# Optimization experiments

Measured on AMD Instinct MI355X. Metric: run time of the kernel, lower is better.

Reference implementation:

```python
import math
import jax, jax.numpy as jnp
import numpy as np

NUM_BUCKETS = 32
MAX_DISTANCE = 128
N_HEADS = 16
D_KV = 64


def _relative_position_bucket(rel_pos):
    # encoder (bidirectional) path of UMT5Attention._relative_position_bucket
    num_buckets = NUM_BUCKETS // 2
    rel_buckets = (rel_pos > 0).astype(jnp.int32) * num_buckets
    rel_pos = jnp.abs(rel_pos)
    max_exact = num_buckets // 2
    is_small = rel_pos < max_exact
    # clamp to 1 inside log only to avoid nan; those entries are masked by is_small
    rel_pos_large = max_exact + (
        jnp.log(jnp.maximum(rel_pos, 1).astype(jnp.float32) / max_exact)
        / math.log(MAX_DISTANCE / max_exact)
        * (num_buckets - max_exact)
    ).astype(jnp.int32)
    rel_pos_large = jnp.minimum(rel_pos_large, num_buckets - 1)
    return rel_buckets + jnp.where(is_small, rel_pos, rel_pos_large)


def compute_bias(rel_bias, q_len, k_len):
    ctx = jnp.arange(q_len, dtype=jnp.int32)[:, None]
    mem = jnp.arange(k_len, dtype=jnp.int32)[None, :]
    bkt = _relative_position_bucket(mem - ctx)          # [q, k]
    values = rel_bias[bkt]                               # [q, k, H]
    return jnp.transpose(values, (2, 0, 1))[None]        # [1, H, q, k]


def setup_inputs() -> dict:
    key = jax.random.key(0)
    ks = jax.random.split(key, 6)
    B, S, D = 2, 2048, 1024
    s = 1.0 / math.sqrt(D)
    return {
        "hidden_states": jax.random.normal(ks[0], (B, S, D), jnp.float32),
        "attention_mask": jnp.ones((B, S), jnp.int32),
        "Wq": jax.random.normal(ks[1], (D, D), jnp.float32) * s,
        "Wk": jax.random.normal(ks[2], (D, D), jnp.float32) * s,
        "Wv": jax.random.normal(ks[3], (D, D), jnp.float32) * s,
        "Wo": jax.random.normal(ks[4], (D, D), jnp.float32) * s,
        "rel_bias": jax.random.normal(ks[5], (NUM_BUCKETS, N_HEADS), jnp.float32),
    }


def reference(hidden_states, attention_mask, Wq, Wk, Wv, Wo, rel_bias):
    b, s, _ = hidden_states.shape
    n, c = N_HEADS, D_KV
    q = (hidden_states @ Wq).reshape(b, s, n, c)
    k = (hidden_states @ Wk).reshape(b, s, n, c)
    v = (hidden_states @ Wv).reshape(b, s, n, c)
    position_bias = compute_bias(rel_bias, s, s)          # [1, H, s, s]
    mask = attention_mask[:, None, None, :]               # [b, 1, 1, s]
    position_bias = jnp.where(mask == 0,
                              jnp.finfo(hidden_states.dtype).min,
                              position_bias)
    # T5-style: no 1/sqrt(d) query scaling
    attn = jnp.einsum('binc,bjnc->bnij', q, k) + position_bias
    attn = jax.nn.softmax(attn, axis=-1)
    o = jnp.einsum('bnij,bjnc->binc', attn, v).reshape(b, s, n * c)
    return o @ Wo
```

## Files before the change

kernel.cpp:

```cpp
#include <hip/hip_runtime.h>
#include <hip/hip_bf16.h>

#define NH 16
#define DC 64
#define SEQ 2048
#define BATCH 2
#define DM 1024
#define MTOT (BATCH*SEQ)

#define LOG2E 1.44269504f
#define SMAX_BOUND 48.0f

typedef unsigned short u16;
typedef unsigned int u32;
typedef __bf16 bf16x8 __attribute__((ext_vector_type(8)));
typedef float f32x4 __attribute__((ext_vector_type(4)));
typedef int i32x4 __attribute__((ext_vector_type(4)));
typedef unsigned u32x2v __attribute__((ext_vector_type(2)));

struct __attribute__((packed, aligned(4))) f4u { f32x4 v; };

__device__ __forceinline__ u16 f2bf(float f) {
    unsigned int x = __float_as_uint(f);
    unsigned int r = (x + 0x7fffu + ((x >> 16) & 1u)) >> 16;
    return (u16)r;
}
__device__ __forceinline__ u32 cvtpk(float a, float b) {
    u32 r;
    asm("v_cvt_pk_bf16_f32 %0, %1, %2" : "=v"(r) : "v"(a), "v"(b));
    return r;
}

__device__ __forceinline__ f32x4 mfma16(bf16x8 a, bf16x8 b, f32x4 c) {
    return __builtin_amdgcn_mfma_f32_16x16x32_bf16(a, b, c, 0, 0, 0);
}

__device__ __forceinline__ void glds(const u16* g, u16* l) {
    __builtin_amdgcn_global_load_lds(
        (const __attribute__((address_space(1))) void*)g,
        (__attribute__((address_space(3))) void*)l, 16, 0, 0);
}

__device__ __forceinline__ float psum32(float v) {
    u32x2v t = __builtin_amdgcn_permlane32_swap(__float_as_uint(v), __float_as_uint(v), false, false);
    return __uint_as_float(t.x) + __uint_as_float(t.y);
}
__device__ __forceinline__ float psum16(float v) {
    u32x2v t = __builtin_amdgcn_permlane16_swap(__float_as_uint(v), __float_as_uint(v), false, false);
    return __uint_as_float(t.x) + __uint_as_float(t.y);
}


__global__ void convert_hs(const float* __restrict__ src, u16* __restrict__ dst, int n4) {
    int idx = blockIdx.x * blockDim.x + threadIdx.x;
    int stride = gridDim.x * blockDim.x;
    for (int i = idx; i < n4; i += stride) {
        float4 v = reinterpret_cast<const float4*>(src)[i];
        uint2 o;
        o.x = (unsigned)f2bf(v.x) | ((unsigned)f2bf(v.y) << 16);
        o.y = (unsigned)f2bf(v.z) | ((unsigned)f2bf(v.w) << 16);
        reinterpret_cast<uint2*>(dst)[i] = o;
    }
}

__global__ void wtrans(const float* __restrict__ Wq, const float* __restrict__ Wk,
                       const float* __restrict__ Wv, const float* __restrict__ Wo,
                       u16* __restrict__ wT) {
    int z = blockIdx.z;
    const float* W = (z == 0) ? Wq : (z == 1) ? Wk : (z == 2) ? Wv : Wo;
    float sc = (z == 0) ? LOG2E : 1.0f;
    u16* WT = wT + (size_t)z * DM * DM;
    __shared__ float tile[32][33];
    int tx = threadIdx.x, ty = threadIdx.y;
    int kbase = blockIdx.y * 32, nbase = blockIdx.x * 32;
#pragma unroll
    for (int i = 0; i < 4; i++)
        tile[ty * 4 + i][tx] = W[(size_t)(kbase + ty * 4 + i) * DM + nbase + tx];
    __syncthreads();
#pragma unroll
    for (int i = 0; i < 4; i++)
        WT[(size_t)(nbase + ty * 4 + i) * DM + kbase + tx] = f2bf(tile[tx][ty * 4 + i] * sc);
}

__global__ void bias_table(const float* __restrict__ rel_bias, float* __restrict__ tab) {
    int idx = blockIdx.x * blockDim.x + threadIdx.x;
    if (idx >= NH * 2 * SEQ) return;
    int n = idx >> 12;
    int dpos = idx & 4095;
    int delta = dpos - 2048;
    int rb = (delta > 0) ? 16 : 0;
    int a = (delta < 0) ? -delta : delta;
    int ib;
    if (a < 8) {
        ib = a;
    } else {
        ib = 8 + (int)(logf((float)a / 8.0f) / logf(16.0f) * 8.0f);
        if (ib > 15) ib = 15;
    }
    tab[idx] = (rel_bias[(rb + ib) * NH + n] - SMAX_BOUND) * LOG2E;
}

__global__ __launch_bounds__(256) void vtrans(const u16* __restrict__ V, u16* __restrict__ VT) {
    int st = blockIdx.x;
    int hb = blockIdx.y;
    const u16* src = V + ((size_t)hb * SEQ + st * 64) * DC;
    u16* dst = VT + (size_t)hb * DC * SEQ + st * 64;
    __shared__ u16 t[64][65];
    int tid = threadIdx.x;
    int r = tid >> 2, c0 = (tid & 3) * 16;
    union { bf16x8 v; u16 s[8]; } a0, a1;
    a0.v = *reinterpret_cast<const bf16x8*>(src + (size_t)r * DC + c0);
    a1.v = *reinterpret_cast<const bf16x8*>(src + (size_t)r * DC + c0 + 8);
#pragma unroll
    for (int j = 0; j < 8; j++) { t[r][c0 + j] = a0.s[j]; t[r][c0 + 8 + j] = a1.s[j]; }
    __syncthreads();
    int c = tid >> 2, s0 = (tid & 3) * 16;
    union { bf16x8 v; u16 s[8]; } o0, o1;
#pragma unroll
    for (int j = 0; j < 8; j++) { o0.s[j] = t[s0 + j][c]; o1.s[j] = t[s0 + 8 + j][c]; }
    *reinterpret_cast<bf16x8*>(dst + (size_t)c * SEQ + s0)     = o0.v;
    *reinterpret_cast<bf16x8*>(dst + (size_t)c * SEQ + s0 + 8) = o1.v;
}


template<int MODE>
__global__ __launch_bounds__(256) void gemm_bt(
    const u16* __restrict__ A, const u16* __restrict__ BT,
    u16* __restrict__ qkvout, float* __restrict__ fout)
{
    const int NTILES = DM / 128;
    const int MTILES = MTOT / 128;
    __shared__ u16 As[128 * 32];
    __shared__ u16 Bs[128 * 32];

    int nb8 = gridDim.x >> 3;
    int bid = (blockIdx.x & 7) * nb8 + (blockIdx.x >> 3);

    int proj = 0, mt, nt;
    if (MODE == 0) {
        proj = bid / (MTILES * NTILES);
        int r = bid % (MTILES * NTILES);
        mt = r / NTILES; nt = r % NTILES;
    } else {
        mt = bid / NTILES; nt = bid % NTILES;
    }
    const u16* Bp = BT + (size_t)proj * DM * DM;
    int m0 = mt * 128, n0 = nt * 128;
    int tid = threadIdx.x;
    int lane = tid & 63, wid = tid >> 6;
    int wrow = (wid >> 1) * 64, wcol = (wid & 1) * 64;

    f32x4 acc[4][4] = {};

    int srow = lane >> 2;
    int skoff = (lane & 3) * 8;

    for (int k0 = 0; k0 < DM; k0 += 32) {
        __syncthreads();
#pragma unroll
        for (int t = 0; t < 2; t++) {
            int chunk = wid * 2 + t;
            int row = chunk * 16 + srow;
            glds(A + (size_t)(m0 + row) * DM + k0 + skoff, &As[chunk * 512]);
        }
#pragma unroll
        for (int t = 0; t < 2; t++) {
            int chunk = wid * 2 + t;
            int row = chunk * 16 + srow;
            glds(Bp + (size_t)(n0 + row) * DM + k0 + skoff, &Bs[chunk * 512]);
        }
        __syncthreads();

        int ko = (lane >> 4) * 8;
        bf16x8 af[4], bfr[4];
#pragma unroll
        for (int mi = 0; mi < 4; mi++)
            af[mi] = *reinterpret_cast<const bf16x8*>(&As[(wrow + mi * 16 + (lane & 15)) * 32 + ko]);
#pragma unroll
        for (int ni = 0; ni < 4; ni++)
            bfr[ni] = *reinterpret_cast<const bf16x8*>(&Bs[(wcol + ni * 16 + (lane & 15)) * 32 + ko]);
#pragma unroll
        for (int mi = 0; mi < 4; mi++)
#pragma unroll
            for (int ni = 0; ni < 4; ni++)
                acc[mi][ni] = mfma16(af[mi], bfr[ni], acc[mi][ni]);
    }

    int rbase = (lane >> 4) * 4;
    int cidx = lane & 15;
#pragma unroll
    for (int mi = 0; mi < 4; mi++) {
#pragma unroll
        for (int ni = 0; ni < 4; ni++) {
#pragma unroll
            for (int r = 0; r < 4; r++) {
                int gm = m0 + wrow + mi * 16 + rbase + r;
                int gn = n0 + wcol + ni * 16 + cidx;
                float v = acc[mi][ni][r];
                if (MODE == 0) {
                    int b = gm >> 11, s = gm & (SEQ - 1);
                    int h = gn >> 6, c = gn & 63;
                    size_t off = (((size_t)b * NH + h) * SEQ + s) * DC + c;
                    qkvout[(size_t)proj * MTOT * DM + off] = f2bf(v);
                } else {
                    fout[(size_t)gm * DM + gn] = v;
                }
            }
        }
    }
}


__global__ __launch_bounds__(256) void attn_kernel(
    const u16* __restrict__ Q, const u16* __restrict__ K, const u16* __restrict__ VT,
    const int* __restrict__ mask, const float* __restrict__ btab,
    u16* __restrict__ O)
{
    __shared__ u16 smem[16384];

    int wg = blockIdx.x;
    int sw = (wg & 7) * 64 + (wg >> 3);
    int qt = sw & 15;
    int bh = sw >> 4;
    int h = bh & 15, b = bh >> 4;

    int tid = threadIdx.x, lane = tid & 63, wid = tid >> 6;
    int q15 = lane & 15, hi = lane >> 4;

    const u16* Qp  = Q  + (((size_t)b * NH + h) * SEQ) * DC;
    const u16* Kp  = K  + (((size_t)b * NH + h) * SEQ) * DC;
    const u16* VTp = VT + ((size_t)b * NH + h) * DC * SEQ;

    int qb = qt * 128 + wid * 32;
    int iq0 = qb + q15;
    int iq1 = qb + 16 + q15;

    bf16x8 qf00 = *reinterpret_cast<const bf16x8*>(Qp + (size_t)iq0 * DC + hi * 8);
    bf16x8 qf01 = *reinterpret_cast<const bf16x8*>(Qp + (size_t)iq0 * DC + 32 + hi * 8);
    bf16x8 qf10 = *reinterpret_cast<const bf16x8*>(Qp + (size_t)iq1 * DC + hi * 8);
    bf16x8 qf11 = *reinterpret_cast<const bf16x8*>(Qp + (size_t)iq1 * DC + 32 + hi * 8);

    int n0 = (wid * 2 + 0) * 64 + lane;
    int n1 = (wid * 2 + 1) * 64 + lane;
    int rA = n0 >> 3, rB = n1 >> 3;
    const u16* gK0 = Kp  + (size_t)rA * DC + (((n0 & 7) ^ (rA & 7)) * 8);
    const u16* gK1 = Kp  + (size_t)rB * DC + (((n1 & 7) ^ (rB & 7)) * 8);
    const u16* gV0 = VTp + (size_t)rA * SEQ + (((n0 & 7) ^ (rA & 7)) * 8);
    const u16* gV1 = VTp + (size_t)rB * SEQ + (((n1 & 7) ^ (rB & 7)) * 8);

    int x0 = (hi)     ^ (q15 & 7);
    int x1 = (hi + 4) ^ (q15 & 7);

    const float* bp0 = btab + (size_t)h * 2 * SEQ + 2048 + hi * 4 - iq0;
    const float* bp1 = bp0 - 16;
    const int* mkp = mask + (size_t)b * SEQ + hi * 4;

    float l0 = 0.0f, l1 = 0.0f;
    f32x4 oacc[4][2] = {};

    glds(gK0, &smem[(wid * 2 + 0) * 512]);
    glds(gK1, &smem[(wid * 2 + 1) * 512]);
    glds(gV0, &smem[4096 + (wid * 2 + 0) * 512]);
    glds(gV1, &smem[4096 + (wid * 2 + 1) * 512]);

#pragma unroll 1
    for (int t = 0; t < SEQ / 64; t++) {
        u16* KsT = smem + ((t & 1) << 13);
        u16* VsT = KsT + 4096;
        int kt = t * 64;

        f32x4 bv0[4], bv1[4]; i32x4 mv4[4];
#pragma unroll
        for (int kf = 0; kf < 4; kf++) {
            bv0[kf] = reinterpret_cast<const f4u*>(bp0 + kt + kf * 16)->v;
            bv1[kf] = reinterpret_cast<const f4u*>(bp1 + kt + kf * 16)->v;
            mv4[kf] = *reinterpret_cast<const i32x4*>(mkp + kt + kf * 16);
        }

        if (t < SEQ / 64 - 1) {
            u16* KsN = smem + (((t + 1) & 1) << 13);
            int aK = (t + 1) * 64 * DC;
            int aV = (t + 1) * 64;
            glds(gK0 + aK, &KsN[(wid * 2 + 0) * 512]);
            glds(gK1 + aK, &KsN[(wid * 2 + 1) * 512]);
            glds(gV0 + aV, &KsN[4096 + (wid * 2 + 0) * 512]);
            glds(gV1 + aV, &KsN[4096 + (wid * 2 + 1) * 512]);
            asm volatile("s_waitcnt vmcnt(4)" ::: "memory");
        } else {
            asm volatile("s_waitcnt vmcnt(0)" ::: "memory");
        }
        asm volatile("s_barrier" ::: "memory");

        f32x4 s0[4], s1[4];
        __builtin_amdgcn_s_setprio(1);
#pragma unroll
        for (int kf = 0; kf < 4; kf++) {
            bf16x8 ka0 = *reinterpret_cast<const bf16x8*>(&KsT[(kf * 16 + q15) * 64 + x0 * 8]);
            bf16x8 ka1 = *reinterpret_cast<const bf16x8*>(&KsT[(kf * 16 + q15) * 64 + x1 * 8]);
            f32x4 z0 = {};
            z0 = mfma16(ka0, qf00, z0);
            z0 = mfma16(ka1, qf01, z0);
            s0[kf] = z0;
            f32x4 z1 = {};
            z1 = mfma16(ka0, qf10, z1);
            z1 = mfma16(ka1, qf11, z1);
            s1[kf] = z1;
        }
        __builtin_amdgcn_s_setprio(0);

#pragma unroll
        for (int kf = 0; kf < 4; kf++) {
#pragma unroll
            for (int r = 0; r < 4; r++) {
                bool mv = (mv4[kf][r] != 0);
                float sv0 = s0[kf][r] + (mv ? bv0[kf][r] : -1e30f);
                float sv1 = s1[kf][r] + (mv ? bv1[kf][r] : -1e30f);
                float p0 = exp2f(sv0);
                float p1 = exp2f(sv1);
                s0[kf][r] = p0; l0 += p0;
                s1[kf][r] = p1; l1 += p1;
            }
        }

        bf16x8 pa00, pa01, pa10, pa11;
        {
            u32 c00 = cvtpk(s0[0][0], s0[0][1]);
            u32 c01 = cvtpk(s0[0][2], s0[0][3]);
            u32 c10 = cvtpk(s0[1][0], s0[1][1]);
            u32 c11 = cvtpk(s0[1][2], s0[1][3]);
            u32 c20 = cvtpk(s0[2][0], s0[2][1]);
            u32 c21 = cvtpk(s0[2][2], s0[2][3]);
            u32 c30 = cvtpk(s0[3][0], s0[3][1]);
            u32 c31 = cvtpk(s0[3][2], s0[3][3]);
            u32x2v t0 = __builtin_amdgcn_permlane32_swap(c00, c10, false, false); c00 = t0.x; c10 = t0.y;
            u32x2v t1 = __builtin_amdgcn_permlane32_swap(c01, c11, false, false); c01 = t1.x; c11 = t1.y;
            u32x2v t2 = __builtin_amdgcn_permlane32_swap(c20, c30, false, false); c20 = t2.x; c30 = t2.y;
            u32x2v t3 = __builtin_amdgcn_permlane32_swap(c21, c31, false, false); c21 = t3.x; c31 = t3.y;
            u32x2v t4 = __builtin_amdgcn_permlane16_swap(c00, c10, false, false); c00 = t4.x; c10 = t4.y;
            u32x2v t5 = __builtin_amdgcn_permlane16_swap(c01, c11, false, false); c01 = t5.x; c11 = t5.y;
            u32x2v t6 = __builtin_amdgcn_permlane16_swap(c20, c30, false, false); c20 = t6.x; c30 = t6.y;
            u32x2v t7 = __builtin_amdgcn_permlane16_swap(c21, c31, false, false); c21 = t7.x; c31 = t7.y;
            union { u32 w[4]; bf16x8 v; } up0, up1;
            up0.w[0] = c00; up0.w[1] = c01; up0.w[2] = c10; up0.w[3] = c11;
            up1.w[0] = c20; up1.w[1] = c21; up1.w[2] = c30; up1.w[3] = c31;
            pa00 = up0.v; pa01 = up1.v;
        }
        {
            u32 c00 = cvtpk(s1[0][0], s1[0][1]);
            u32 c01 = cvtpk(s1[0][2], s1[0][3]);
            u32 c10 = cvtpk(s1[1][0], s1[1][1]);
            u32 c11 = cvtpk(s1[1][2], s1[1][3]);
            u32 c20 = cvtpk(s1[2][0], s1[2][1]);
            u32 c21 = cvtpk(s1[2][2], s1[2][3]);
            u32 c30 = cvtpk(s1[3][0], s1[3][1]);
            u32 c31 = cvtpk(s1[3][2], s1[3][3]);
            u32x2v t0 = __builtin_amdgcn_permlane32_swap(c00, c10, false, false); c00 = t0.x; c10 = t0.y;
            u32x2v t1 = __builtin_amdgcn_permlane32_swap(c01, c11, false, false); c01 = t1.x; c11 = t1.y;
            u32x2v t2 = __builtin_amdgcn_permlane32_swap(c20, c30, false, false); c20 = t2.x; c30 = t2.y;
            u32x2v t3 = __builtin_amdgcn_permlane32_swap(c21, c31, false, false); c21 = t3.x; c31 = t3.y;
            u32x2v t4 = __builtin_amdgcn_permlane16_swap(c00, c10, false, false); c00 = t4.x; c10 = t4.y;
            u32x2v t5 = __builtin_amdgcn_permlane16_swap(c01, c11, false, false); c01 = t5.x; c11 = t5.y;
            u32x2v t6 = __builtin_amdgcn_permlane16_swap(c20, c30, false, false); c20 = t6.x; c30 = t6.y;
            u32x2v t7 = __builtin_amdgcn_permlane16_swap(c21, c31, false, false); c21 = t7.x; c31 = t7.y;
            union { u32 w[4]; bf16x8 v; } up0, up1;
            up0.w[0] = c00; up0.w[1] = c01; up0.w[2] = c10; up0.w[3] = c11;
            up1.w[0] = c20; up1.w[1] = c21; up1.w[2] = c30; up1.w[3] = c31;
            pa10 = up0.v; pa11 = up1.v;
        }

        __builtin_amdgcn_s_setprio(1);
#pragma unroll
        for (int ci = 0; ci < 4; ci++) {
            bf16x8 v0 = *reinterpret_cast<const bf16x8*>(&VsT[(ci * 16 + q15) * 64 + x0 * 8]);
            bf16x8 v1 = *reinterpret_cast<const bf16x8*>(&VsT[(ci * 16 + q15) * 64 + x1 * 8]);
            oacc[ci][0] = mfma16(v0, pa00, oacc[ci][0]);
            oacc[ci][0] = mfma16(v1, pa01, oacc[ci][0]);
            oacc[ci][1] = mfma16(v0, pa10, oacc[ci][1]);
            oacc[ci][1] = mfma16(v1, pa11, oacc[ci][1]);
        }
        __builtin_amdgcn_s_setprio(0);

        asm volatile("s_barrier" ::: "memory");
    }

    float rl0 = 1.0f / psum16(psum32(l0));
    float rl1 = 1.0f / psum16(psum32(l1));
    __syncthreads();
    u16* Ot = smem;
#pragma unroll
    for (int ci = 0; ci < 4; ci++) {
        u32 w00 = cvtpk(oacc[ci][0][0] * rl0, oacc[ci][0][1] * rl0);
        u32 w01 = cvtpk(oacc[ci][0][2] * rl0, oacc[ci][0][3] * rl0);
        int base0 = (wid * 32 + q15) * 72 + ci * 16 + hi * 4;
        *reinterpret_cast<u32*>(&Ot[base0])     = w00;
        *reinterpret_cast<u32*>(&Ot[base0 + 2]) = w01;
        u32 w10 = cvtpk(oacc[ci][1][0] * rl1, oacc[ci][1][1] * rl1);
        u32 w11 = cvtpk(oacc[ci][1][2] * rl1, oacc[ci][1][3] * rl1);
        int base1 = (wid * 32 + 16 + q15) * 72 + ci * 16 + hi * 4;
        *reinterpret_cast<u32*>(&Ot[base1])     = w10;
        *reinterpret_cast<u32*>(&Ot[base1 + 2]) = w11;
    }
    __syncthreads();
    int row = tid >> 1, part = tid & 1;
    bf16x8 o0 = *reinterpret_cast<const bf16x8*>(&Ot[row * 72 + part * 32]);
    bf16x8 o1 = *reinterpret_cast<const bf16x8*>(&Ot[row * 72 + part * 32 + 8]);
    bf16x8 o2 = *reinterpret_cast<const bf16x8*>(&Ot[row * 72 + part * 32 + 16]);
    bf16x8 o3 = *reinterpret_cast<const bf16x8*>(&Ot[row * 72 + part * 32 + 24]);
    size_t ob = ((size_t)b * SEQ + qt * 128 + row) * DM + h * DC + part * 32;
    *reinterpret_cast<bf16x8*>(&O[ob])      = o0;
    *reinterpret_cast<bf16x8*>(&O[ob + 8])  = o1;
    *reinterpret_cast<bf16x8*>(&O[ob + 16]) = o2;
    *reinterpret_cast<bf16x8*>(&O[ob + 24]) = o3;
}


extern "C" void kernel_launch(void* const* d_in, const int* in_sizes, int n_in,
                              void* d_out, int out_size, void* d_ws, size_t ws_size,
                              hipStream_t stream) {
    const float* hs   = (const float*)d_in[0];
    const int*   mask = (const int*)d_in[1];
    const float* Wq   = (const float*)d_in[2];
    const float* Wk   = (const float*)d_in[3];
    const float* Wv   = (const float*)d_in[4];
    const float* Wo   = (const float*)d_in[5];
    const float* rb   = (const float*)d_in[6];

    char* ws = (char*)d_ws;
    u16* hsb  = (u16*)(ws);
    u16* wT   = (u16*)(ws + 8388608);
    u16* Qb   = (u16*)(ws + 16777216);
    u16* Ob   = (u16*)(ws + 41943040);
    float* btab = (float*)(ws + 50331648);
    float* out = (float*)d_out;

    u16* VT = hsb;

    convert_hs<<<2048, 256, 0, stream>>>(hs, hsb, MTOT * DM / 4);
    wtrans<<<dim3(32, 32, 4), dim3(32, 8), 0, stream>>>(Wq, Wk, Wv, Wo, wT);
    bias_table<<<256, 256, 0, stream>>>(rb, btab);
    gemm_bt<0><<<768, 256, 0, stream>>>(hsb, wT, Qb, nullptr);
    vtrans<<<dim3(32, 32), 256, 0, stream>>>(Qb + 2 * (size_t)MTOT * DM, VT);
    attn_kernel<<<512, 256, 0, stream>>>(
        Qb, Qb + (size_t)MTOT * DM, VT, mask, btab, Ob);
    gemm_bt<1><<<256, 256, 0, stream>>>(Ob, wT + 3 * (size_t)DM * DM, nullptr, out);
}
```

Baseline: 149.4 us.

## Split attention key tiles across wave pairs and merge three prep kernels

The attention kernel now runs 512 threads per block. Each pair of waves shares a 32-row query group and splits each 64-key tile into two halves. Partial output accumulators and row sums are reduced through LDS at the end, and each wave issues only one kind of async load (K or V^T). The three preprocessing kernels (hs conversion, weight transpose, bias table) are fused into one launch. This aims to raise wave-level parallelism and latency hiding in attention and to cut launch overhead, at the cost of an extra LDS reduction and more sync at the end.

```diff
diff --git a/kernel.cpp b/kernel.cpp
--- a/kernel.cpp
+++ b/kernel.cpp
@@ -51,53 +51,57 @@
 }
 
 
-__global__ void convert_hs(const float* __restrict__ src, u16* __restrict__ dst, int n4) {
-    int idx = blockIdx.x * blockDim.x + threadIdx.x;
-    int stride = gridDim.x * blockDim.x;
-    for (int i = idx; i < n4; i += stride) {
-        float4 v = reinterpret_cast<const float4*>(src)[i];
-        uint2 o;
-        o.x = (unsigned)f2bf(v.x) | ((unsigned)f2bf(v.y) << 16);
-        o.y = (unsigned)f2bf(v.z) | ((unsigned)f2bf(v.w) << 16);
-        reinterpret_cast<uint2*>(dst)[i] = o;
-    }
-}
-
-__global__ void wtrans(const float* __restrict__ Wq, const float* __restrict__ Wk,
-                       const float* __restrict__ Wv, const float* __restrict__ Wo,
-                       u16* __restrict__ wT) {
-    int z = blockIdx.z;
-    const float* W = (z == 0) ? Wq : (z == 1) ? Wk : (z == 2) ? Wv : Wo;
-    float sc = (z == 0) ? LOG2E : 1.0f;
-    u16* WT = wT + (size_t)z * DM * DM;
-    __shared__ float tile[32][33];
-    int tx = threadIdx.x, ty = threadIdx.y;
-    int kbase = blockIdx.y * 32, nbase = blockIdx.x * 32;
-#pragma unroll
-    for (int i = 0; i < 4; i++)
-        tile[ty * 4 + i][tx] = W[(size_t)(kbase + ty * 4 + i) * DM + nbase + tx];
-    __syncthreads();
-#pragma unroll
-    for (int i = 0; i < 4; i++)
-        WT[(size_t)(nbase + ty * 4 + i) * DM + kbase + tx] = f2bf(tile[tx][ty * 4 + i] * sc);
-}
-
-__global__ void bias_table(const float* __restrict__ rel_bias, float* __restrict__ tab) {
-    int idx = blockIdx.x * blockDim.x + threadIdx.x;
-    if (idx >= NH * 2 * SEQ) return;
-    int n = idx >> 12;
-    int dpos = idx & 4095;
-    int delta = dpos - 2048;
-    int rb = (delta > 0) ? 16 : 0;
-    int a = (delta < 0) ? -delta : delta;
-    int ib;
-    if (a < 8) {
-        ib = a;
+__global__ __launch_bounds__(256) void prep_kernel(
+    const float* __restrict__ hs,
+    const float* __restrict__ Wq, const float* __restrict__ Wk,
+    const float* __restrict__ Wv, const float* __restrict__ Wo,
+    const float* __restrict__ rel_bias,
+    u16* __restrict__ hsb, u16* __restrict__ wT, float* __restrict__ btab)
+{
+    int bid = blockIdx.x, tid = threadIdx.x;
+    if (bid < 4096) {
+        int z = bid >> 10, rem = bid & 1023;
+        int by = rem >> 5, bx = rem & 31;
+        const float* W = (z == 0) ? Wq : (z == 1) ? Wk : (z == 2) ? Wv : Wo;
+        float sc = (z == 0) ? LOG2E : 1.0f;
+        u16* WT = wT + (size_t)z * DM * DM;
+        __shared__ float tile[32][33];
+        int tx = tid & 31, ty = tid >> 5;
+        int kbase = by * 32, nbase = bx * 32;
+#pragma unroll
+        for (int i = 0; i < 4; i++)
+            tile[ty * 4 + i][tx] = W[(size_t)(kbase + ty * 4 + i) * DM + nbase + tx];
+        __syncthreads();
+#pragma unroll
+        for (int i = 0; i < 4; i++)
+            WT[(size_t)(nbase + ty * 4 + i) * DM + kbase + tx] = f2bf(tile[tx][ty * 4 + i] * sc);
+    } else if (bid < 6144) {
+        int idx = (bid - 4096) * 256 + tid;
+        int stride = 2048 * 256;
+        int n4 = MTOT * DM / 4;
+        for (int i = idx; i < n4; i += stride) {
+            float4 v = reinterpret_cast<const float4*>(hs)[i];
+            uint2 o;
+            o.x = (unsigned)f2bf(v.x) | ((unsigned)f2bf(v.y) << 16);
+            o.y = (unsigned)f2bf(v.z) | ((unsigned)f2bf(v.w) << 16);
+            reinterpret_cast<uint2*>(hsb)[i] = o;
+        }
     } else {
-        ib = 8 + (int)(logf((float)a / 8.0f) / logf(16.0f) * 8.0f);
-        if (ib > 15) ib = 15;
-    }
-    tab[idx] = (rel_bias[(rb + ib) * NH + n] - SMAX_BOUND) * LOG2E;
+        int idx = (bid - 6144) * 256 + tid;
+        int n = idx >> 12;
+        int dpos = idx & 4095;
+        int delta = dpos - 2048;
+        int rb = (delta > 0) ? 16 : 0;
+        int a = (delta < 0) ? -delta : delta;
+        int ib;
+        if (a < 8) {
+            ib = a;
+        } else {
+            ib = 8 + (int)(logf((float)a / 8.0f) / logf(16.0f) * 8.0f);
+            if (ib > 15) ib = 15;
+        }
+        btab[idx] = (rel_bias[(rb + ib) * NH + n] - SMAX_BOUND) * LOG2E;
+    }
 }
 
 __global__ __launch_bounds__(256) void vtrans(const u16* __restrict__ V, u16* __restrict__ VT) {
@@ -211,12 +215,13 @@
 }
 
 
-__global__ __launch_bounds__(256) void attn_kernel(
+__global__ __launch_bounds__(512, 4) void attn_kernel(
     const u16* __restrict__ Q, const u16* __restrict__ K, const u16* __restrict__ VT,
     const int* __restrict__ mask, const float* __restrict__ btab,
     u16* __restrict__ O)
 {
     __shared__ u16 smem[16384];
+    __shared__ float lds_l[4][2][16];
 
     int wg = blockIdx.x;
     int sw = (wg & 7) * 64 + (wg >> 3);
@@ -226,12 +231,13 @@
 
     int tid = threadIdx.x, lane = tid & 63, wid = tid >> 6;
     int q15 = lane & 15, hi = lane >> 4;
+    int qg = wid >> 1, kh = wid & 1;
 
     const u16* Qp  = Q  + (((size_t)b * NH + h) * SEQ) * DC;
     const u16* Kp  = K  + (((size_t)b * NH + h) * SEQ) * DC;
     const u16* VTp = VT + ((size_t)b * NH + h) * DC * SEQ;
 
-    int qb = qt * 128 + wid * 32;
+    int qb = qt * 128 + qg * 32;
     int iq0 = qb + q15;
     int iq1 = qb + 16 + q15;
 
@@ -240,28 +246,32 @@
     bf16x8 qf10 = *reinterpret_cast<const bf16x8*>(Qp + (size_t)iq1 * DC + hi * 8);
     bf16x8 qf11 = *reinterpret_cast<const bf16x8*>(Qp + (size_t)iq1 * DC + 32 + hi * 8);
 
-    int n0 = (wid * 2 + 0) * 64 + lane;
-    int n1 = (wid * 2 + 1) * 64 + lane;
-    int rA = n0 >> 3, rB = n1 >> 3;
-    const u16* gK0 = Kp  + (size_t)rA * DC + (((n0 & 7) ^ (rA & 7)) * 8);
-    const u16* gK1 = Kp  + (size_t)rB * DC + (((n1 & 7) ^ (rB & 7)) * 8);
-    const u16* gV0 = VTp + (size_t)rA * SEQ + (((n0 & 7) ^ (rA & 7)) * 8);
-    const u16* gV1 = VTp + (size_t)rB * SEQ + (((n1 & 7) ^ (rB & 7)) * 8);
-
-    int x0 = (hi)     ^ (q15 & 7);
-    int x1 = (hi + 4) ^ (q15 & 7);
-
-    const float* bp0 = btab + (size_t)h * 2 * SEQ + 2048 + hi * 4 - iq0;
+    int c0 = wid * 2, c1 = wid * 2 + 1;
+    int lr0 = (c0 & 7) * 8 + (lane >> 3);
+    int lr1 = (c1 & 7) * 8 + (lane >> 3);
+    int cc0 = (lane & 7) ^ (lr0 & 7);
+    int cc1 = (lane & 7) ^ (lr1 & 7);
+    const u16* g0 = (wid < 4) ? (Kp + (size_t)lr0 * DC + cc0 * 8)
+                              : (VTp + (size_t)lr0 * SEQ + cc0 * 8);
+    const u16* g1 = (wid < 4) ? (Kp + (size_t)lr1 * DC + cc1 * 8)
+                              : (VTp + (size_t)lr1 * SEQ + cc1 * 8);
+    int adv = (wid < 4) ? 64 * DC : 64;
+    u16* ldst0 = &smem[c0 * 512];
+    u16* ldst1 = &smem[c1 * 512];
+
+    int x0 = (hi)         ^ (q15 & 7);
+    int x1 = (hi + 4)     ^ (q15 & 7);
+    int xv = (kh * 4 + hi) ^ (q15 & 7);
+
+    const float* bp0 = btab + (size_t)h * 2 * SEQ + 2048 + kh * 32 + hi * 4 - iq0;
     const float* bp1 = bp0 - 16;
-    const int* mkp = mask + (size_t)b * SEQ + hi * 4;
+    const int* mkp = mask + (size_t)b * SEQ + kh * 32 + hi * 4;
 
     float l0 = 0.0f, l1 = 0.0f;
     f32x4 oacc[4][2] = {};
 
-    glds(gK0, &smem[(wid * 2 + 0) * 512]);
-    glds(gK1, &smem[(wid * 2 + 1) * 512]);
-    glds(gV0, &smem[4096 + (wid * 2 + 0) * 512]);
-    glds(gV1, &smem[4096 + (wid * 2 + 1) * 512]);
+    glds(g0, ldst0);
+    glds(g1, ldst1);
 
 #pragma unroll 1
     for (int t = 0; t < SEQ / 64; t++) {
@@ -269,34 +279,31 @@
         u16* VsT = KsT + 4096;
         int kt = t * 64;
 
-        f32x4 bv0[4], bv1[4]; i32x4 mv4[4];
-#pragma unroll
-        for (int kf = 0; kf < 4; kf++) {
+        f32x4 bv0[2], bv1[2]; i32x4 mv4[2];
+#pragma unroll
+        for (int kf = 0; kf < 2; kf++) {
             bv0[kf] = reinterpret_cast<const f4u*>(bp0 + kt + kf * 16)->v;
             bv1[kf] = reinterpret_cast<const f4u*>(bp1 + kt + kf * 16)->v;
             mv4[kf] = *reinterpret_cast<const i32x4*>(mkp + kt + kf * 16);
         }
 
         if (t < SEQ / 64 - 1) {
-            u16* KsN = smem + (((t + 1) & 1) << 13);
-            int aK = (t + 1) * 64 * DC;
-            int aV = (t + 1) * 64;
-            glds(gK0 + aK, &KsN[(wid * 2 + 0) * 512]);
-            glds(gK1 + aK, &KsN[(wid * 2 + 1) * 512]);
-            glds(gV0 + aV, &KsN[4096 + (wid * 2 + 0) * 512]);
-            glds(gV1 + aV, &KsN[4096 + (wid * 2 + 1) * 512]);
-            asm volatile("s_waitcnt vmcnt(4)" ::: "memory");
+            u16* nb = smem + (((t + 1) & 1) << 13);
+            glds(g0 + (size_t)(t + 1) * adv, &nb[c0 * 512]);
+            glds(g1 + (size_t)(t + 1) * adv, &nb[c1 * 512]);
+            asm volatile("s_waitcnt vmcnt(2)" ::: "memory");
         } else {
             asm volatile("s_waitcnt vmcnt(0)" ::: "memory");
         }
         asm volatile("s_barrier" ::: "memory");
 
-        f32x4 s0[4], s1[4];
+        f32x4 s0[2], s1[2];
         __builtin_amdgcn_s_setprio(1);
 #pragma unroll
-        for (int kf = 0; kf < 4; kf++) {
-            bf16x8 ka0 = *reinterpret_cast<const bf16x8*>(&KsT[(kf * 16 + q15) * 64 + x0 * 8]);
-            bf16x8 ka1 = *reinterpret_cast<const bf16x8*>(&KsT[(kf * 16 + q15) * 64 + x1 * 8]);
+        for (int kf = 0; kf < 2; kf++) {
+            int row = ((kh * 2 + kf) * 16 + q15) * 64;
+            bf16x8 ka0 = *reinterpret_cast<const bf16x8*>(&KsT[row + x0 * 8]);
+            bf16x8 ka1 = *reinterpret_cast<const bf16x8*>(&KsT[row + x1 * 8]);
             f32x4 z0 = {};
             z0 = mfma16(ka0, qf00, z0);
             z0 = mfma16(ka1, qf01, z0);
@@ -309,7 +316,7 @@
         __builtin_amdgcn_s_setprio(0);
 
 #pragma unroll
-        for (int kf = 0; kf < 4; kf++) {
+        for (int kf = 0; kf < 2; kf++) {
 #pragma unroll
             for (int r = 0; r < 4; r++) {
                 bool mv = (mv4[kf][r] != 0);
@@ -322,95 +329,96 @@
             }
         }
 
-        bf16x8 pa00, pa01, pa10, pa11;
+        bf16x8 pa0, pa1;
         {
-            u32 c00 = cvtpk(s0[0][0], s0[0][1]);
-            u32 c01 = cvtpk(s0[0][2], s0[0][3]);
-            u32 c10 = cvtpk(s0[1][0], s0[1][1]);
-            u32 c11 = cvtpk(s0[1][2], s0[1][3]);
-            u32 c20 = cvtpk(s0[2][0], s0[2][1]);
-            u32 c21 = cvtpk(s0[2][2], s0[2][3]);
-            u32 c30 = cvtpk(s0[3][0], s0[3][1]);
-            u32 c31 = cvtpk(s0[3][2], s0[3][3]);
-            u32x2v t0 = __builtin_amdgcn_permlane32_swap(c00, c10, false, false); c00 = t0.x; c10 = t0.y;
-            u32x2v t1 = __builtin_amdgcn_permlane32_swap(c01, c11, false, false); c01 = t1.x; c11 = t1.y;
-            u32x2v t2 = __builtin_amdgcn_permlane32_swap(c20, c30, false, false); c20 = t2.x; c30 = t2.y;
-            u32x2v t3 = __builtin_amdgcn_permlane32_swap(c21, c31, false, false); c21 = t3.x; c31 = t3.y;
-            u32x2v t4 = __builtin_amdgcn_permlane16_swap(c00, c10, false, false); c00 = t4.x; c10 = t4.y;
-            u32x2v t5 = __builtin_amdgcn_permlane16_swap(c01, c11, false, false); c01 = t5.x; c11 = t5.y;
-            u32x2v t6 = __builtin_amdgcn_permlane16_swap(c20, c30, false, false); c20 = t6.x; c30 = t6.y;
-            u32x2v t7 = __builtin_amdgcn_permlane16_swap(c21, c31, false, false); c21 = t7.x; c31 = t7.y;
-            union { u32 w[4]; bf16x8 v; } up0, up1;
-            up0.w[0] = c00; up0.w[1] = c01; up0.w[2] = c10; up0.w[3] = c11;
-            up1.w[0] = c20; up1.w[1] = c21; up1.w[2] = c30; up1.w[3] = c31;
-            pa00 = up0.v; pa01 = up1.v;
+            u32 cA0 = cvtpk(s0[0][0], s0[0][1]);
+            u32 cA1 = cvtpk(s0[0][2], s0[0][3]);
+            u32 cB0 = cvtpk(s0[1][0], s0[1][1]);
+            u32 cB1 = cvtpk(s0[1][2], s0[1][3]);
+            u32x2v t0 = __builtin_amdgcn_permlane32_swap(cA0, cB0, false, false);
+            u32x2v t1 = __builtin_amdgcn_permlane32_swap(cA1, cB1, false, false);
+            u32x2v t2 = __builtin_amdgcn_permlane16_swap(t0.x, t0.y, false, false);
+            u32x2v t3 = __builtin_amdgcn_permlane16_swap(t1.x, t1.y, false, false);
+            union { u32 w[4]; bf16x8 v; } up;
+            up.w[0] = t2.x; up.w[1] = t3.x; up.w[2] = t2.y; up.w[3] = t3.y;
+            pa0 = up.v;
         }
         {
-            u32 c00 = cvtpk(s1[0][0], s1[0][1]);
-            u32 c01 = cvtpk(s1[0][2], s1[0][3]);
-            u32 c10 = cvtpk(s1[1][0], s1[1][1]);
-            u32 c11 = cvtpk(s1[1][2], s1[1][3]);
-            u32 c20 = cvtpk(s1[2][0], s1[2][1]);
-            u32 c21 = cvtpk(s1[2][2], s1[2][3]);
-            u32 c30 = cvtpk(s1[3][0], s1[3][1]);
-            u32 c31 = cvtpk(s1[3][2], s1[3][3]);
-            u32x2v t0 = __builtin_amdgcn_permlane32_swap(c00, c10, false, false); c00 = t0.x; c10 = t0.y;
-            u32x2v t1 = __builtin_amdgcn_permlane32_swap(c01, c11, false, false); c01 = t1.x; c11 = t1.y;
-            u32x2v t2 = __builtin_amdgcn_permlane32_swap(c20, c30, false, false); c20 = t2.x; c30 = t2.y;
-            u32x2v t3 = __builtin_amdgcn_permlane32_swap(c21, c31, false, false); c21 = t3.x; c31 = t3.y;
-            u32x2v t4 = __builtin_amdgcn_permlane16_swap(c00, c10, false, false); c00 = t4.x; c10 = t4.y;
-            u32x2v t5 = __builtin_amdgcn_permlane16_swap(c01, c11, false, false); c01 = t5.x; c11 = t5.y;
-            u32x2v t6 = __builtin_amdgcn_permlane16_swap(c20, c30, false, false); c20 = t6.x; c30 = t6.y;
-            u32x2v t7 = __builtin_amdgcn_permlane16_swap(c21, c31, false, false); c21 = t7.x; c31 = t7.y;
-            union { u32 w[4]; bf16x8 v; } up0, up1;
-            up0.w[0] = c00; up0.w[1] = c01; up0.w[2] = c10; up0.w[3] = c11;
-            up1.w[0] = c20; up1.w[1] = c21; up1.w[2] = c30; up1.w[3] = c31;
-            pa10 = up0.v; pa11 = up1.v;
+            u32 cA0 = cvtpk(s1[0][0], s1[0][1]);
+            u32 cA1 = cvtpk(s1[0][2], s1[0][3]);
+            u32 cB0 = cvtpk(s1[1][0], s1[1][1]);
+            u32 cB1 = cvtpk(s1[1][2], s1[1][3]);
+            u32x2v t0 = __builtin_amdgcn_permlane32_swap(cA0, cB0, false, false);
+            u32x2v t1 = __builtin_amdgcn_permlane32_swap(cA1, cB1, false, false);
+            u32x2v t2 = __builtin_amdgcn_permlane16_swap(t0.x, t0.y, false, false);
+            u32x2v t3 = __builtin_amdgcn_permlane16_swap(t1.x, t1.y, false, false);
+            union { u32 w[4]; bf16x8 v; } up;
+            up.w[0] = t2.x; up.w[1] = t3.x; up.w[2] = t2.y; up.w[3] = t3.y;
+            pa1 = up.v;
         }
 
         __builtin_amdgcn_s_setprio(1);
 #pragma unroll
         for (int ci = 0; ci < 4; ci++) {
-            bf16x8 v0 = *reinterpret_cast<const bf16x8*>(&VsT[(ci * 16 + q15) * 64 + x0 * 8]);
-            bf16x8 v1 = *reinterpret_cast<const bf16x8*>(&VsT[(ci * 16 + q15) * 64 + x1 * 8]);
-            oacc[ci][0] = mfma16(v0, pa00, oacc[ci][0]);
-            oacc[ci][0] = mfma16(v1, pa01, oacc[ci][0]);
-            oacc[ci][1] = mfma16(v0, pa10, oacc[ci][1]);
-            oacc[ci][1] = mfma16(v1, pa11, oacc[ci][1]);
+            bf16x8 vf = *reinterpret_cast<const bf16x8*>(&VsT[(ci * 16 + q15) * 64 + xv * 8]);
+            oacc[ci][0] = mfma16(vf, pa0, oacc[ci][0]);
+            oacc[ci][1] = mfma16(vf, pa1, oacc[ci][1]);
         }
         __builtin_amdgcn_s_setprio(0);
 
         asm volatile("s_barrier" ::: "memory");
     }
 
-    float rl0 = 1.0f / psum16(psum32(l0));
-    float rl1 = 1.0f / psum16(psum32(l1));
+    l0 = psum16(psum32(l0));
+    l1 = psum16(psum32(l1));
     __syncthreads();
+
+    float* fs = reinterpret_cast<float*>(smem);
+    if (kh == 1) {
+#pragma unroll
+        for (int ci = 0; ci < 4; ci++)
+#pragma unroll
+            for (int qs = 0; qs < 2; qs++)
+                *reinterpret_cast<f32x4*>(&fs[qg * 2048 + (ci * 2 + qs) * 256 + lane * 4]) = oacc[ci][qs];
+        if (hi == 0) { lds_l[qg][0][q15] = l0; lds_l[qg][1][q15] = l1; }
+    }
+    __syncthreads();
+
+    float rl0 = 0.0f, rl1 = 0.0f;
+    if (kh == 0) {
+#pragma unroll
+        for (int ci = 0; ci < 4; ci++)
+#pragma unroll
+            for (int qs = 0; qs < 2; qs++)
+                oacc[ci][qs] += *reinterpret_cast<const f32x4*>(&fs[qg * 2048 + (ci * 2 + qs) * 256 + lane * 4]);
+        rl0 = 1.0f / (l0 + lds_l[qg][0][q15]);
+        rl1 = 1.0f / (l1 + lds_l[qg][1][q15]);
+    }
+    __syncthreads();
+
     u16* Ot = smem;
-#pragma unroll
-    for (int ci = 0; ci < 4; ci++) {
-        u32 w00 = cvtpk(oacc[ci][0][0] * rl0, oacc[ci][0][1] * rl0);
-        u32 w01 = cvtpk(oacc[ci][0][2] * rl0, oacc[ci][0][3] * rl0);
-        int base0 = (wid * 32 + q15) * 72 + ci * 16 + hi * 4;
-        *reinterpret_cast<u32*>(&Ot[base0])     = w00;
-        *reinterpret_cast<u32*>(&Ot[base0 + 2]) = w01;
-        u32 w10 = cvtpk(oacc[ci][1][0] * rl1, oacc[ci][1][1] * rl1);
-        u32 w11 = cvtpk(oacc[ci][1][2] * rl1, oacc[ci][1][3] * rl1);
-        int base1 = (wid * 32 + 16 + q15) * 72 + ci * 16 + hi * 4;
-        *reinterpret_cast<u32*>(&Ot[base1])     = w10;
-        *reinterpret_cast<u32*>(&Ot[base1 + 2]) = w11;
+    if (kh == 0) {
+#pragma unroll
+        for (int ci = 0; ci < 4; ci++) {
+            u32 w00 = cvtpk(oacc[ci][0][0] * rl0, oacc[ci][0][1] * rl0);
+            u32 w01 = cvtpk(oacc[ci][0][2] * rl0, oacc[ci][0][3] * rl0);
+            int base0 = (qg * 32 + q15) * 72 + ci * 16 + hi * 4;
+            *reinterpret_cast<u32*>(&Ot[base0])     = w00;
+            *reinterpret_cast<u32*>(&Ot[base0 + 2]) = w01;
+            u32 w10 = cvtpk(oacc[ci][1][0] * rl1, oacc[ci][1][1] * rl1);
+            u32 w11 = cvtpk(oacc[ci][1][2] * rl1, oacc[ci][1][3] * rl1);
+            int base1 = (qg * 32 + 16 + q15) * 72 + ci * 16 + hi * 4;
+            *reinterpret_cast<u32*>(&Ot[base1])     = w10;
+            *reinterpret_cast<u32*>(&Ot[base1 + 2]) = w11;
+        }
     }
     __syncthreads();
-    int row = tid >> 1, part = tid & 1;
-    bf16x8 o0 = *reinterpret_cast<const bf16x8*>(&Ot[row * 72 + part * 32]);
-    bf16x8 o1 = *reinterpret_cast<const bf16x8*>(&Ot[row * 72 + part * 32 + 8]);
-    bf16x8 o2 = *reinterpret_cast<const bf16x8*>(&Ot[row * 72 + part * 32 + 16]);
-    bf16x8 o3 = *reinterpret_cast<const bf16x8*>(&Ot[row * 72 + part * 32 + 24]);
-    size_t ob = ((size_t)b * SEQ + qt * 128 + row) * DM + h * DC + part * 32;
-    *reinterpret_cast<bf16x8*>(&O[ob])      = o0;
-    *reinterpret_cast<bf16x8*>(&O[ob + 8])  = o1;
-    *reinterpret_cast<bf16x8*>(&O[ob + 16]) = o2;
-    *reinterpret_cast<bf16x8*>(&O[ob + 24]) = o3;
+    int row = tid >> 2, part = tid & 3;
+    bf16x8 o0 = *reinterpret_cast<const bf16x8*>(&Ot[row * 72 + part * 16]);
+    bf16x8 o1 = *reinterpret_cast<const bf16x8*>(&Ot[row * 72 + part * 16 + 8]);
+    size_t ob = ((size_t)b * SEQ + qt * 128 + row) * DM + h * DC + part * 16;
+    *reinterpret_cast<bf16x8*>(&O[ob])     = o0;
+    *reinterpret_cast<bf16x8*>(&O[ob + 8]) = o1;
 }
 
 
@@ -435,12 +443,10 @@
 
     u16* VT = hsb;
 
-    convert_hs<<<2048, 256, 0, stream>>>(hs, hsb, MTOT * DM / 4);
-    wtrans<<<dim3(32, 32, 4), dim3(32, 8), 0, stream>>>(Wq, Wk, Wv, Wo, wT);
-    bias_table<<<256, 256, 0, stream>>>(rb, btab);
+    prep_kernel<<<6400, 256, 0, stream>>>(hs, Wq, Wk, Wv, Wo, rb, hsb, wT, btab);
     gemm_bt<0><<<768, 256, 0, stream>>>(hsb, wT, Qb, nullptr);
     vtrans<<<dim3(32, 32), 256, 0, stream>>>(Qb + 2 * (size_t)MTOT * DM, VT);
-    attn_kernel<<<512, 256, 0, stream>>>(
+    attn_kernel<<<512, 512, 0, stream>>>(
         Qb, Qb + (size_t)MTOT * DM, VT, mask, btab, Ob);
     gemm_bt<1><<<256, 256, 0, stream>>>(Ob, wT + 3 * (size_t)DM * DM, nullptr, out);
 }
```

After: 148.1 us. Within noise of the previous version (-0.9%).
